# Performance work log

Measured on AMD Instinct MI355X. Metric: run time of the kernel, lower is better.

The kernel has to match this reference:

```python
import jax, jax.numpy as jnp
import numpy as np

DIN = 1024
DOUT = 1024
NUM_HEAD = 16
HEAD_DIM = DIN // NUM_HEAD  # 64
SEQ = 2048
BS = 4


def setup_inputs() -> dict:
    key = jax.random.key(0)
    ks = jax.random.split(key, 9)
    s_in = 1.0 / np.sqrt(DIN)
    s_out = 1.0 / np.sqrt(DOUT)
    return {
        "x": jax.random.normal(ks[0], (BS, SEQ, DIN), dtype=jnp.float32),
        "Wq": jax.random.normal(ks[1], (DIN, DOUT), dtype=jnp.float32) * s_in,
        "bq": jax.random.normal(ks[2], (DOUT,), dtype=jnp.float32) * s_in,
        "Wk": jax.random.normal(ks[3], (DIN, DOUT), dtype=jnp.float32) * s_in,
        "bk": jax.random.normal(ks[4], (DOUT,), dtype=jnp.float32) * s_in,
        "Wv": jax.random.normal(ks[5], (DIN, DOUT), dtype=jnp.float32) * s_in,
        "bv": jax.random.normal(ks[6], (DOUT,), dtype=jnp.float32) * s_in,
        "Wo": jax.random.normal(ks[7], (DOUT, DOUT), dtype=jnp.float32) * s_out,
        "bo": jax.random.normal(ks[8], (DOUT,), dtype=jnp.float32) * s_out,
    }


def reference(x, Wq, bq, Wk, bk, Wv, bv, Wo, bo):
    bs, n, _ = x.shape
    # projections -> [bs, n, H, hd] -> [bs, H, n, hd]
    def split_heads(t):
        return t.reshape(bs, n, NUM_HEAD, HEAD_DIM).transpose(0, 2, 1, 3)

    q = split_heads(x @ Wq + bq)
    k = split_heads(x @ Wk + bk)
    v = split_heads(x @ Wv + bv)

    # full [bs, H, n, n] scores, causal mask, scaled softmax
    scores = jnp.einsum("bhqd,bhkd->bhqk", q, k)
    causal = jnp.tril(jnp.ones((n, n), dtype=bool))
    scores = jnp.where(causal, scores, -jnp.inf)
    att = jax.nn.softmax(scores / np.sqrt(HEAD_DIM), axis=-1)

    ctx = jnp.einsum("bhqk,bhkd->bhqd", att, v)
    ctx = ctx.transpose(0, 2, 1, 3).reshape(bs, n, DOUT)
    return ctx @ Wo + bo
```

## Files before the change

### kernel.cpp

```cpp
#include <hip/hip_runtime.h>
#include <hip/hip_bf16.h>
#include <stdint.h>

#define DIN   1024
#define DOUT  1024
#define NHEAD 16
#define HDIM  64
#define SEQL  2048
#define BSZ   4
#define MTOT  (BSZ*SEQL)
#define KDIM  1024

typedef __bf16 bf16x8 __attribute__((ext_vector_type(8)));
typedef float  f32x4  __attribute__((ext_vector_type(4)));

__device__ __forceinline__ f32x4 mfma16(bf16x8 a, bf16x8 b, f32x4 c) {
    return __builtin_amdgcn_mfma_f32_16x16x32_bf16(a, b, c, 0, 0, 0);
}

__device__ __forceinline__ void gl_lds16(const void* gsrc, void* ldst) {
    __builtin_amdgcn_global_load_lds(
        (const __attribute__((address_space(1))) uint32_t*)gsrc,
        (__attribute__((address_space(3))) uint32_t*)ldst, 16, 0, 0);
}

#if __has_builtin(__builtin_amdgcn_exp2f)
__device__ __forceinline__ float fexp2(float x) { return __builtin_amdgcn_exp2f(x); }
#else
__device__ __forceinline__ float fexp2(float x) { return exp2f(x); }
#endif

__device__ __forceinline__ unsigned int cvtpk(float lo, float hi) {
    unsigned int r;
    asm("v_cvt_pk_bf16_f32 %0, %1, %2" : "=v"(r) : "v"(lo), "v"(hi));
    return r;
}

__device__ __forceinline__ unsigned int pk_bf16(float lo, float hi) {
    unsigned int a = __float_as_uint(lo);
    unsigned int b = __float_as_uint(hi);
    a += 0x7FFFu + ((a >> 16) & 1u);
    b += 0x7FFFu + ((b >> 16) & 1u);
    return __builtin_amdgcn_perm(b, a, 0x07060302u);
}

__global__ void cvt_bf16(const float4* __restrict__ in, uint2* __restrict__ out, int n4) {
    int idx = blockIdx.x * blockDim.x + threadIdx.x;
    int stride = gridDim.x * blockDim.x;
    for (int i = idx; i < n4; i += stride) {
        float4 v = in[i];
        uint2 o;
        o.x = pk_bf16(v.x, v.y);
        o.y = pk_bf16(v.z, v.w);
        out[i] = o;
    }
}

__global__ void transpose_cvt3(const float* __restrict__ W0, const float* __restrict__ W1,
                               const float* __restrict__ W2, __hip_bfloat16* __restrict__ Wt3) {
    __shared__ __hip_bfloat16 t[32][33];
    const int tx = threadIdx.x, ty = threadIdx.y;
    const int bx = blockIdx.x, by = blockIdx.y, z = blockIdx.z;
    const float* W = (z == 0) ? W0 : (z == 1) ? W1 : W2;
    __hip_bfloat16* Wt = Wt3 + (size_t)z * DOUT * DIN;
#pragma unroll
    for (int r = 0; r < 4; ++r)
        t[ty + 8*r][tx] = __float2bfloat16(W[(size_t)(by*32 + ty + 8*r) * DOUT + bx*32 + tx]);
    __syncthreads();
#pragma unroll
    for (int r = 0; r < 4; ++r)
        Wt[(size_t)(bx*32 + ty + 8*r) * DIN + by*32 + tx] = t[tx][ty + 8*r];
}

__global__ void transpose_cvt(const float* __restrict__ W, __hip_bfloat16* __restrict__ Wt) {
    __shared__ __hip_bfloat16 t[32][33];
    const int tx = threadIdx.x, ty = threadIdx.y;
    const int bx = blockIdx.x, by = blockIdx.y;
#pragma unroll
    for (int r = 0; r < 4; ++r)
        t[ty + 8*r][tx] = __float2bfloat16(W[(size_t)(by*32 + ty + 8*r) * DOUT + bx*32 + tx]);
    __syncthreads();
#pragma unroll
    for (int r = 0; r < 4; ++r)
        Wt[(size_t)(bx*32 + ty + 8*r) * DIN + by*32 + tx] = t[tx][ty + 8*r];
}

template <int EPI>
__global__ __launch_bounds__(256)
void gemm_mfma(const __hip_bfloat16* __restrict__ A,
               const __hip_bfloat16* __restrict__ Bt,
               const float* __restrict__ b0, const float* __restrict__ b1,
               void* __restrict__ o0, void* __restrict__ o1,
               float scale)
{
    __shared__ alignas(16) __hip_bfloat16 As[2][4][128][8];
    __shared__ alignas(16) __hip_bfloat16 Bs[2][4][128][8];

    const int tid  = threadIdx.x;
    const int w    = tid >> 6;
    const int lane = tid & 63;
    const int g    = lane >> 4;
    const int r    = lane & 15;
    const int wr   = w >> 1, wc = w & 1;

    int bx = blockIdx.x, by = blockIdx.y;
    {
        const int gx    = gridDim.x;
        const int total = gx * gridDim.y;
        const int flat  = bx + gx * by;
        const int nf    = (flat & 7) * (total >> 3) + (flat >> 3);
        by = nf / gx;
        bx = nf % gx;
    }
    const int row0 = by * 128;
    const int col0 = bx * 128;

    f32x4 acc[4][4];
#pragma unroll
    for (int m = 0; m < 4; ++m)
#pragma unroll
        for (int n = 0; n < 4; ++n) acc[m][n] = (f32x4)0.0f;

    auto stage = [&](int buf, int kt) {
        const __hip_bfloat16* ga = A  + (size_t)(row0 + lane) * KDIM + kt*32 + 8*w;
        const __hip_bfloat16* gb = Bt + (size_t)(col0 + lane) * KDIM + kt*32 + 8*w;
        gl_lds16(ga,            &As[buf][w][0][0]);
        gl_lds16(ga + 64*KDIM,  &As[buf][w][64][0]);
        gl_lds16(gb,            &Bs[buf][w][0][0]);
        gl_lds16(gb + 64*KDIM,  &Bs[buf][w][64][0]);
    };

    stage(0, 0);
    __syncthreads();

    const int NKT = KDIM / 32;
    for (int kt = 0; kt < NKT; ++kt) {
        const int cur = kt & 1;
        if (kt + 1 < NKT) stage(cur ^ 1, kt + 1);

        bf16x8 af[4], bfr[4];
#pragma unroll
        for (int m = 0; m < 4; ++m)
            af[m] = *reinterpret_cast<const bf16x8*>(&As[cur][g][64*wr + 16*m + r][0]);
#pragma unroll
        for (int n = 0; n < 4; ++n)
            bfr[n] = *reinterpret_cast<const bf16x8*>(&Bs[cur][g][64*wc + 16*n + r][0]);

#pragma unroll
        for (int m = 0; m < 4; ++m)
#pragma unroll
            for (int n = 0; n < 4; ++n) {
                if (EPI == 1) acc[m][n] = mfma16(af[m], bfr[n], acc[m][n]);
                else          acc[m][n] = mfma16(bfr[n], af[m], acc[m][n]);
            }

        __syncthreads();
    }

    if (EPI == 0) {
        const int slab = col0 >> 10;
        const float* bp = (slab == 0) ? b0 : b1;
        __hip_bfloat16* op = (__hip_bfloat16*)((slab == 0) ? o0 : o1);
        const float sc = (slab == 0) ? scale : 1.0f;
#pragma unroll
        for (int m = 0; m < 4; ++m) {
            const int rowg = row0 + 64*wr + 16*m + r;
            const int bb = rowg >> 11, sq = rowg & (SEQL-1);
#pragma unroll
            for (int n = 0; n < 4; ++n) {
                const int c2 = (col0 & 1023) + 64*wc + 16*n + 4*g;
                const int hh = c2 >> 6, dd = c2 & (HDIM-1);
                const float4 bv4 = *reinterpret_cast<const float4*>(&bp[c2]);
                uint2 ov;
                ov.x = pk_bf16((acc[m][n][0] + bv4.x) * sc, (acc[m][n][1] + bv4.y) * sc);
                ov.y = pk_bf16((acc[m][n][2] + bv4.z) * sc, (acc[m][n][3] + bv4.w) * sc);
                *reinterpret_cast<uint2*>(
                    &op[(((size_t)(bb*NHEAD + hh) * SEQL + sq) << 6) + dd]) = ov;
            }
        }
    } else if (EPI == 1) {
#pragma unroll
        for (int n = 0; n < 4; ++n) {
            const int colg = col0 + 64*wc + 16*n + r;
            const int hh = colg >> 6, dd = colg & (HDIM-1);
            const float bv_ = b0[colg];
#pragma unroll
            for (int m = 0; m < 4; ++m) {
                const int rowg0 = row0 + 64*wr + 16*m + 4*g;
                const int bb = rowg0 >> 11, sq0 = rowg0 & (SEQL-1);
                uint2 ov;
                ov.x = pk_bf16(acc[m][n][0] + bv_, acc[m][n][1] + bv_);
                ov.y = pk_bf16(acc[m][n][2] + bv_, acc[m][n][3] + bv_);
                *reinterpret_cast<uint2*>(
                    &((__hip_bfloat16*)o0)[((size_t)(bb*NHEAD + hh) * HDIM + dd) * SEQL + sq0]) = ov;
            }
        }
    } else {
#pragma unroll
        for (int m = 0; m < 4; ++m) {
            const int rowg = row0 + 64*wr + 16*m + r;
#pragma unroll
            for (int n = 0; n < 4; ++n) {
                const int colg0 = col0 + 64*wc + 16*n + 4*g;
                const float4 bv4 = *reinterpret_cast<const float4*>(&b0[colg0]);
                float4 ov;
                ov.x = acc[m][n][0] + bv4.x;
                ov.y = acc[m][n][1] + bv4.y;
                ov.z = acc[m][n][2] + bv4.z;
                ov.w = acc[m][n][3] + bv4.w;
                *reinterpret_cast<float4*>(&((float*)o0)[(size_t)rowg * DOUT + colg0]) = ov;
            }
        }
    }
}

__global__ __launch_bounds__(256)
void attn_fwd(const __hip_bfloat16* __restrict__ Q,
              const __hip_bfloat16* __restrict__ K,
              const __hip_bfloat16* __restrict__ Vt,
              __hip_bfloat16* __restrict__ ctx)
{
    __shared__ alignas(16) __hip_bfloat16 Ps[4][2][16][64];
    __shared__ alignas(16) f32x4 Om[2][64][8];
    __shared__ float Ml[2][64][5];

    const int tid  = threadIdx.x;
    const int w    = tid >> 6;
    const int lane = tid & 63;
    const int g    = lane >> 4;
    const int r    = lane & 15;
    const int swz  = (r & 7) << 3;
    const int pp   = w >> 1;
    const int half = w & 1;

    const int bh = blockIdx.x;
    const int b  = bh >> 4, h = bh & 15;

    const __hip_bfloat16* Qh = Q  + (size_t)bh * SEQL * HDIM;
    const __hip_bfloat16* Kh = K  + (size_t)bh * SEQL * HDIM;
    const __hip_bfloat16* Vh = Vt + (size_t)bh * HDIM * SEQL;

    const int sp = blockIdx.y * 2 + pp;

#pragma unroll 1
    for (int ti = 0; ti < 2; ++ti) {
        const int strip = ti ? (63 - sp) : sp;
        const int qb = strip * 32;

        bf16x8 qf[2][2];
#pragma unroll
        for (int m = 0; m < 2; ++m)
#pragma unroll
            for (int hh = 0; hh < 2; ++hh)
                qf[m][hh] = *reinterpret_cast<const bf16x8*>(
                    Qh + (size_t)(qb + 16*m + r) * HDIM + 32*hh + 8*g);

        f32x4 o[2][4];
        float mrow[2], lrow[2];
#pragma unroll
        for (int m = 0; m < 2; ++m) {
#pragma unroll
            for (int n = 0; n < 4; ++n) o[m][n] = (f32x4)0.0f;
            mrow[m] = -1e30f; lrow[m] = 0.0f;
        }

        const int nst = ((qb + 31) >> 6) + 1;
        const int ns2 = (nst + 1) >> 1;
        const int k0  = half ? ns2 : 0;
        const int k1  = half ? nst : ns2;

        const __hip_bfloat16* kp01 = Kh + (size_t)(k0*64 + r) * HDIM + 8*g;
        const __hip_bfloat16* kp23 = kp01 + 32*HDIM;
        const __hip_bfloat16* vp0  = Vh + (size_t)r * SEQL + (size_t)k0*64 + 8*g;
        const __hip_bfloat16* vp1  = vp0 + (size_t)16*SEQL;
        const __hip_bfloat16* vp2  = vp0 + (size_t)32*SEQL;
        const __hip_bfloat16* vp3  = vp0 + (size_t)48*SEQL;

#pragma unroll 1
        for (int kt = k0; kt < k1; ++kt) {
            const int key0 = kt * 64;

            bf16x8 kf[4][2], vf[4][2];
#pragma unroll
            for (int hh = 0; hh < 2; ++hh) {
                kf[0][hh] = *reinterpret_cast<const bf16x8*>(kp01 + hh*32);
                kf[1][hh] = *reinterpret_cast<const bf16x8*>(kp01 + 16*HDIM + hh*32);
                kf[2][hh] = *reinterpret_cast<const bf16x8*>(kp23 + hh*32);
                kf[3][hh] = *reinterpret_cast<const bf16x8*>(kp23 + 16*HDIM + hh*32);
                vf[0][hh] = *reinterpret_cast<const bf16x8*>(vp0 + hh*32);
                vf[1][hh] = *reinterpret_cast<const bf16x8*>(vp1 + hh*32);
                vf[2][hh] = *reinterpret_cast<const bf16x8*>(vp2 + hh*32);
                vf[3][hh] = *reinterpret_cast<const bf16x8*>(vp3 + hh*32);
            }
            kp01 += 64*HDIM; kp23 += 64*HDIM;
            vp0 += 64; vp1 += 64; vp2 += 64; vp3 += 64;

            f32x4 s[2][4];
            __builtin_amdgcn_s_setprio(1);
#pragma unroll
            for (int m = 0; m < 2; ++m)
#pragma unroll
                for (int c = 0; c < 4; ++c) {
                    f32x4 t = (f32x4)0.0f;
                    t = mfma16(kf[c][0], qf[m][0], t);
                    t = mfma16(kf[c][1], qf[m][1], t);
                    s[m][c] = t;
                }
            __builtin_amdgcn_s_setprio(0);

            if (kt == nst - 1) {
#pragma unroll
                for (int m = 0; m < 2; ++m) {
                    const int qrow = qb + 16*m + r;
#pragma unroll
                    for (int c = 0; c < 4; ++c) {
                        const int kb = key0 + 16*c + 4*g;
#pragma unroll
                        for (int j = 0; j < 4; ++j)
                            if (kb + j > qrow) s[m][c][j] = -1e30f;
                    }
                }
            }

#pragma unroll
            for (int m = 0; m < 2; ++m) {
                float t0 = fmaxf(fmaxf(s[m][0][0], s[m][0][1]), fmaxf(s[m][0][2], s[m][0][3]));
                float t1 = fmaxf(fmaxf(s[m][1][0], s[m][1][1]), fmaxf(s[m][1][2], s[m][1][3]));
                float t2 = fmaxf(fmaxf(s[m][2][0], s[m][2][1]), fmaxf(s[m][2][2], s[m][2][3]));
                float t3 = fmaxf(fmaxf(s[m][3][0], s[m][3][1]), fmaxf(s[m][3][2], s[m][3][3]));
                float pml = fmaxf(fmaxf(t0, t1), fmaxf(t2, t3));

                if (__any(pml > mrow[m] + 11.0f)) {
                    float pm = fmaxf(pml, __shfl_xor(pml, 16));
                    pm = fmaxf(pm, __shfl_xor(pm, 32));
                    const float mnew = fmaxf(mrow[m], pm);
                    const float fac  = fexp2(mrow[m] - mnew);
                    mrow[m] = mnew;
                    lrow[m] *= fac;
#pragma unroll
                    for (int n = 0; n < 4; ++n) o[m][n] *= fac;
                }

                float p[4][4];
#pragma unroll
                for (int c = 0; c < 4; ++c)
#pragma unroll
                    for (int j = 0; j < 4; ++j)
                        p[c][j] = fexp2(s[m][c][j] - mrow[m]);

                float u0 = (p[0][0] + p[0][1]) + (p[0][2] + p[0][3]);
                float u1 = (p[1][0] + p[1][1]) + (p[1][2] + p[1][3]);
                float u2 = (p[2][0] + p[2][1]) + (p[2][2] + p[2][3]);
                float u3 = (p[3][0] + p[3][1]) + (p[3][2] + p[3][3]);
                lrow[m] += (u0 + u1) + (u2 + u3);

#pragma unroll
                for (int c = 0; c < 4; ++c) {
                    uint2 pk;
                    pk.x = cvtpk(p[c][0], p[c][1]);
                    pk.y = cvtpk(p[c][2], p[c][3]);
                    *reinterpret_cast<uint2*>(&Ps[w][m][r][(16*c + 4*g) ^ swz]) = pk;
                }
            }

            bf16x8 pf[2][2];
#pragma unroll
            for (int m = 0; m < 2; ++m)
#pragma unroll
                for (int hh = 0; hh < 2; ++hh)
                    pf[m][hh] = *reinterpret_cast<const bf16x8*>(
                        &Ps[w][m][r][(32*hh + 8*g) ^ swz]);

            __builtin_amdgcn_s_setprio(1);
#pragma unroll
            for (int n = 0; n < 4; ++n)
#pragma unroll
                for (int m = 0; m < 2; ++m) {
                    o[m][n] = mfma16(vf[n][0], pf[m][0], o[m][n]);
                    o[m][n] = mfma16(vf[n][1], pf[m][1], o[m][n]);
                }
            __builtin_amdgcn_s_setprio(0);
        }

#pragma unroll
        for (int m = 0; m < 2; ++m) {
            lrow[m] += __shfl_xor(lrow[m], 16);
            lrow[m] += __shfl_xor(lrow[m], 32);
        }

        if (half) {
#pragma unroll
            for (int m = 0; m < 2; ++m)
#pragma unroll
                for (int n = 0; n < 4; ++n)
                    Om[pp][lane][(m*4 + n) ^ (lane & 7)] = o[m][n];
            Ml[pp][lane][0] = mrow[0];
            Ml[pp][lane][1] = mrow[1];
            Ml[pp][lane][2] = lrow[0];
            Ml[pp][lane][3] = lrow[1];
        }
        __syncthreads();
        if (!half) {
#pragma unroll
            for (int m = 0; m < 2; ++m) {
                const float m1 = Ml[pp][lane][m];
                const float l1 = Ml[pp][lane][2 + m];
                const float M  = fmaxf(mrow[m], m1);
                const float f0 = fexp2(mrow[m] - M);
                const float f1 = fexp2(m1 - M);
                const float L  = lrow[m] * f0 + l1 * f1;
                const float inv = 1.0f / L;
                const size_t rowbase = (size_t)(b*SEQL + qb + 16*m + r) * DOUT + h*HDIM;
#pragma unroll
                for (int n = 0; n < 4; ++n) {
                    const f32x4 o1 = Om[pp][lane][(m*4 + n) ^ (lane & 7)];
                    uint2 ov;
                    ov.x = cvtpk((o[m][n][0]*f0 + o1[0]*f1) * inv,
                                 (o[m][n][1]*f0 + o1[1]*f1) * inv);
                    ov.y = cvtpk((o[m][n][2]*f0 + o1[2]*f1) * inv,
                                 (o[m][n][3]*f0 + o1[3]*f1) * inv);
                    *reinterpret_cast<uint2*>(&ctx[rowbase + 16*n + 4*g]) = ov;
                }
            }
        }
        __syncthreads();
    }
}

extern "C" void kernel_launch(void* const* d_in, const int* in_sizes, int n_in,
                              void* d_out, int out_size, void* d_ws, size_t ws_size,
                              hipStream_t stream) {
    const float* x  = (const float*)d_in[0];
    const float* Wq = (const float*)d_in[1];
    const float* bq = (const float*)d_in[2];
    const float* Wk = (const float*)d_in[3];
    const float* bk = (const float*)d_in[4];
    const float* Wv = (const float*)d_in[5];
    const float* bv = (const float*)d_in[6];
    const float* Wo = (const float*)d_in[7];
    const float* bo = (const float*)d_in[8];
    float* out = (float*)d_out;
    (void)in_sizes; (void)n_in; (void)out_size; (void)ws_size;

    char* ws = (char*)d_ws;
    __hip_bfloat16* xb  = (__hip_bfloat16*)ws;
    __hip_bfloat16* Wt3 = (__hip_bfloat16*)(ws + (16u << 20));
    __hip_bfloat16* Wot = (__hip_bfloat16*)(ws + (22u << 20));
    __hip_bfloat16* Qb  = (__hip_bfloat16*)(ws + (24u << 20));
    __hip_bfloat16* Kb  = Qb + (size_t)MTOT * DOUT;
    __hip_bfloat16* Vtb = Kb + (size_t)MTOT * DOUT;
    __hip_bfloat16* ctx = xb;

    cvt_bf16<<<2048, 256, 0, stream>>>((const float4*)x, (uint2*)xb, MTOT * DIN / 4);

    dim3 tb(32, 8);
    transpose_cvt3<<<dim3(32, 32, 3), tb, 0, stream>>>(Wq, Wk, Wv, Wt3);
    transpose_cvt <<<dim3(32, 32),    tb, 0, stream>>>(Wo, Wot);

    dim3 gqk(2*DOUT / 128, MTOT / 128);
    gemm_mfma<0><<<gqk, 256, 0, stream>>>(xb, Wt3, bq, bk, Qb, Kb,
                                          0.125f * 1.44269504088896f);
    dim3 gv(DOUT / 128, MTOT / 128);
    gemm_mfma<1><<<gv, 256, 0, stream>>>(xb, Wt3 + (size_t)2*DOUT*DIN, bv, nullptr,
                                         Vtb, nullptr, 1.0f);

    dim3 ag(BSZ * NHEAD, 16);
    attn_fwd<<<ag, 256, 0, stream>>>(Qb, Kb, Vtb, ctx);

    gemm_mfma<2><<<gv, 256, 0, stream>>>(ctx, Wot, bo, nullptr,
                                         out, nullptr, 1.0f);
}
```

Measured before the change: 306.3 us.

## Prefetch next K tile in attention loop with ping-pong registers; use hardware bf16 pack

In the attention kernel, the K fragments for the next key tile are now loaded into a second register set while the current tile is processed, using a two-way unrolled ping-pong loop, so global load latency overlaps with the MFMA and softmax work. The software round-to-nearest bf16 packing is replaced with the v_cvt_pk_bf16_f32 instruction in the convert and GEMM epilogues. The GEMM block-index swizzle is removed in favour of a direct blockIdx mapping. The extra K register set raises VGPR pressure and could lower occupancy, and dropping the swizzle may change L2 locality.

```diff
diff --git a/kernel.cpp b/kernel.cpp
--- a/kernel.cpp
+++ b/kernel.cpp
@@ -36,22 +36,14 @@
     return r;
 }
 
-__device__ __forceinline__ unsigned int pk_bf16(float lo, float hi) {
-    unsigned int a = __float_as_uint(lo);
-    unsigned int b = __float_as_uint(hi);
-    a += 0x7FFFu + ((a >> 16) & 1u);
-    b += 0x7FFFu + ((b >> 16) & 1u);
-    return __builtin_amdgcn_perm(b, a, 0x07060302u);
-}
-
 __global__ void cvt_bf16(const float4* __restrict__ in, uint2* __restrict__ out, int n4) {
     int idx = blockIdx.x * blockDim.x + threadIdx.x;
     int stride = gridDim.x * blockDim.x;
     for (int i = idx; i < n4; i += stride) {
         float4 v = in[i];
         uint2 o;
-        o.x = pk_bf16(v.x, v.y);
-        o.y = pk_bf16(v.z, v.w);
+        o.x = cvtpk(v.x, v.y);
+        o.y = cvtpk(v.z, v.w);
         out[i] = o;
     }
 }
@@ -103,17 +95,8 @@
     const int r    = lane & 15;
     const int wr   = w >> 1, wc = w & 1;
 
-    int bx = blockIdx.x, by = blockIdx.y;
-    {
-        const int gx    = gridDim.x;
-        const int total = gx * gridDim.y;
-        const int flat  = bx + gx * by;
-        const int nf    = (flat & 7) * (total >> 3) + (flat >> 3);
-        by = nf / gx;
-        bx = nf % gx;
-    }
-    const int row0 = by * 128;
-    const int col0 = bx * 128;
+    const int row0 = blockIdx.y * 128;
+    const int col0 = blockIdx.x * 128;
 
     f32x4 acc[4][4];
 #pragma unroll
@@ -172,8 +155,8 @@
                 const int hh = c2 >> 6, dd = c2 & (HDIM-1);
                 const float4 bv4 = *reinterpret_cast<const float4*>(&bp[c2]);
                 uint2 ov;
-                ov.x = pk_bf16((acc[m][n][0] + bv4.x) * sc, (acc[m][n][1] + bv4.y) * sc);
-                ov.y = pk_bf16((acc[m][n][2] + bv4.z) * sc, (acc[m][n][3] + bv4.w) * sc);
+                ov.x = cvtpk((acc[m][n][0] + bv4.x) * sc, (acc[m][n][1] + bv4.y) * sc);
+                ov.y = cvtpk((acc[m][n][2] + bv4.z) * sc, (acc[m][n][3] + bv4.w) * sc);
                 *reinterpret_cast<uint2*>(
                     &op[(((size_t)(bb*NHEAD + hh) * SEQL + sq) << 6) + dd]) = ov;
             }
@@ -189,8 +172,8 @@
                 const int rowg0 = row0 + 64*wr + 16*m + 4*g;
                 const int bb = rowg0 >> 11, sq0 = rowg0 & (SEQL-1);
                 uint2 ov;
-                ov.x = pk_bf16(acc[m][n][0] + bv_, acc[m][n][1] + bv_);
-                ov.y = pk_bf16(acc[m][n][2] + bv_, acc[m][n][3] + bv_);
+                ov.x = cvtpk(acc[m][n][0] + bv_, acc[m][n][1] + bv_);
+                ov.y = cvtpk(acc[m][n][2] + bv_, acc[m][n][3] + bv_);
                 *reinterpret_cast<uint2*>(
                     &((__hip_bfloat16*)o0)[((size_t)(bb*NHEAD + hh) * HDIM + dd) * SEQL + sq0]) = ov;
             }
@@ -270,30 +253,37 @@
         const int k1  = half ? nst : ns2;
 
         const __hip_bfloat16* kp01 = Kh + (size_t)(k0*64 + r) * HDIM + 8*g;
-        const __hip_bfloat16* kp23 = kp01 + 32*HDIM;
         const __hip_bfloat16* vp0  = Vh + (size_t)r * SEQL + (size_t)k0*64 + 8*g;
         const __hip_bfloat16* vp1  = vp0 + (size_t)16*SEQL;
         const __hip_bfloat16* vp2  = vp0 + (size_t)32*SEQL;
         const __hip_bfloat16* vp3  = vp0 + (size_t)48*SEQL;
 
-#pragma unroll 1
-        for (int kt = k0; kt < k1; ++kt) {
+        bf16x8 kA[4][2], kB[4][2];
+
+        auto loadK = [&](bf16x8 (&kf)[4][2]) __attribute__((always_inline)) {
+#pragma unroll
+            for (int c = 0; c < 4; ++c)
+#pragma unroll
+                for (int hh = 0; hh < 2; ++hh)
+                    kf[c][hh] = *reinterpret_cast<const bf16x8*>(
+                        kp01 + c*16*HDIM + hh*32);
+            kp01 += 64*HDIM;
+        };
+
+        auto step = [&](bf16x8 (&KC)[4][2], bf16x8 (&KN)[4][2], int kt)
+                        __attribute__((always_inline)) {
             const int key0 = kt * 64;
 
-            bf16x8 kf[4][2], vf[4][2];
+            bf16x8 vf[4][2];
 #pragma unroll
             for (int hh = 0; hh < 2; ++hh) {
-                kf[0][hh] = *reinterpret_cast<const bf16x8*>(kp01 + hh*32);
-                kf[1][hh] = *reinterpret_cast<const bf16x8*>(kp01 + 16*HDIM + hh*32);
-                kf[2][hh] = *reinterpret_cast<const bf16x8*>(kp23 + hh*32);
-                kf[3][hh] = *reinterpret_cast<const bf16x8*>(kp23 + 16*HDIM + hh*32);
                 vf[0][hh] = *reinterpret_cast<const bf16x8*>(vp0 + hh*32);
                 vf[1][hh] = *reinterpret_cast<const bf16x8*>(vp1 + hh*32);
                 vf[2][hh] = *reinterpret_cast<const bf16x8*>(vp2 + hh*32);
                 vf[3][hh] = *reinterpret_cast<const bf16x8*>(vp3 + hh*32);
             }
-            kp01 += 64*HDIM; kp23 += 64*HDIM;
             vp0 += 64; vp1 += 64; vp2 += 64; vp3 += 64;
+            if (kt + 1 < k1) loadK(KN);
 
             f32x4 s[2][4];
             __builtin_amdgcn_s_setprio(1);
@@ -302,8 +292,8 @@
 #pragma unroll
                 for (int c = 0; c < 4; ++c) {
                     f32x4 t = (f32x4)0.0f;
-                    t = mfma16(kf[c][0], qf[m][0], t);
-                    t = mfma16(kf[c][1], qf[m][1], t);
+                    t = mfma16(KC[c][0], qf[m][0], t);
+                    t = mfma16(KC[c][1], qf[m][1], t);
                     s[m][c] = t;
                 }
             __builtin_amdgcn_s_setprio(0);
@@ -380,6 +370,13 @@
                     o[m][n] = mfma16(vf[n][1], pf[m][1], o[m][n]);
                 }
             __builtin_amdgcn_s_setprio(0);
+        };
+
+        loadK(kA);
+        int kt = k0;
+        while (kt < k1) {
+            step(kA, kB, kt); if (++kt >= k1) break;
+            step(kB, kA, kt); ++kt;
         }
 
 #pragma unroll
```

Result: slower. 324.4 us (+5.9%).
